# Optimization experiments

Measured on AMD Instinct MI355X. Metric: run time of the kernel, lower is better.

Reference implementation:

```python
import jax, jax.numpy as jnp
import numpy as np

SLOPE = 25.0   # snntorch surrogate.fast_sigmoid default slope
THR = 1.0      # snntorch Leaky default threshold
NUM_STEPS = 100

# fast_sigmoid surrogate spike: heaviside fwd, 1/(slope|x|+1)^2 bwd
@jax.custom_vjp
def spike(x):
    return (x > 0).astype(x.dtype)

def _spike_fwd(x):
    return spike(x), x

def _spike_bwd(x, g):
    return (g / (SLOPE * jnp.abs(x) + 1.0) ** 2,)

spike.defvjp(_spike_fwd, _spike_bwd)


def setup_inputs() -> dict:
    key = jax.random.key(0)
    ks = jax.random.split(key, 5)
    B, D_in, D_h, D_out = 512, 784, 2048, 10
    x = jax.random.normal(ks[0], (B, D_in), dtype=jnp.float32)
    W1 = jax.random.normal(ks[1], (D_h, D_in), dtype=jnp.float32) / np.sqrt(D_in).astype(np.float32)
    b1 = jax.random.normal(ks[2], (D_h,), dtype=jnp.float32) * 0.01
    W2 = jax.random.normal(ks[3], (D_out, D_h), dtype=jnp.float32) / np.sqrt(D_h).astype(np.float32)
    b2 = jax.random.normal(ks[4], (D_out,), dtype=jnp.float32) * 0.01
    beta1 = jnp.asarray(0.9, dtype=jnp.float32)  # learn_beta=True -> parameter
    beta2 = jnp.asarray(0.9, dtype=jnp.float32)
    return {"x": x, "W1": W1, "b1": b1, "W2": W2, "b2": b2, "beta1": beta1, "beta2": beta2}


def reference(x, W1, b1, W2, b2, beta1, beta2):
    dtype = x.dtype
    B = x.shape[0]
    Dh = W1.shape[0]
    Do = W2.shape[0]
    # fc1(x) is loop-invariant in the original (x constant across steps) -> hoist
    cur1 = x @ W1.T + b1                       # [B, Dh]
    b1c = jnp.clip(beta1, 0.0, 1.0)            # snntorch clamps beta in forward
    b2c = jnp.clip(beta2, 0.0, 1.0)
    mem1_0 = jnp.zeros((B, Dh), dtype)         # init_leaky -> 0
    mem2_0 = jnp.zeros((B, Do), dtype)

    def step(carry, _):
        mem1, mem2 = carry
        # snntorch Leaky (reset_mechanism='subtract'):
        # reset_t = detached heaviside(mem_{t-1} - thr); mem_t = beta*mem_{t-1} + cur - reset*thr
        reset1 = jax.lax.stop_gradient((mem1 > THR).astype(dtype))
        mem1 = b1c * mem1 + cur1 - reset1 * THR
        spk1 = spike(mem1 - THR)               # [B, Dh]
        cur2 = spk1 @ W2.T + b2                # [B, Do]
        reset2 = jax.lax.stop_gradient((mem2 > THR).astype(dtype))
        mem2 = b2c * mem2 + cur2 - reset2 * THR
        spk2 = spike(mem2 - THR)
        return (mem1, mem2), spk2

    _, spk2_rec = jax.lax.scan(step, (mem1_0, mem2_0), None, length=NUM_STEPS)  # [T, B, Do]
    # snn_res_step_num == snn_num_steps -> mean over all steps
    stk_mean = jnp.mean(spk2_rec, axis=0)      # [B, Do]
    return jax.nn.softmax(stk_mean, axis=1)
```

## Files before the change

### kernel.cpp

```cpp
#include <hip/hip_runtime.h>
#include <cstdint>

typedef unsigned int u32;
typedef unsigned short u16;
typedef unsigned long long u64;
typedef __attribute__((ext_vector_type(4))) float f32x4;
typedef __attribute__((ext_vector_type(8))) short s16x8;

#define D_IN   784
#define D_H    2048
#define D_O    10
#define T_STEPS 100

static __device__ __forceinline__ u16 f2bf_rn(float f) {
  u32 u = __float_as_uint(f);
  u32 r = u + 0x7FFFu + ((u >> 16) & 1u);
  return (u16)(r >> 16);
}
static __device__ __forceinline__ float bf2f(u16 h) {
  return __uint_as_float(((u32)h) << 16);
}

static __device__ __forceinline__ void packpair(float f0, float f1,
                                                u32& o0, u32& o1, u32& o2) {
  u32 u0 = __float_as_uint(f0), u1 = __float_as_uint(f1);
  o0 = (u0 >> 16) | (u1 & 0xFFFF0000u);
  float r0 = __fsub_rn(f0, __uint_as_float(u0 & 0xFFFF0000u));
  float r1 = __fsub_rn(f1, __uint_as_float(u1 & 0xFFFF0000u));
  u32 v0 = __float_as_uint(r0), v1 = __float_as_uint(r1);
  o1 = (v0 >> 16) | (v1 & 0xFFFF0000u);
  float s0 = __fsub_rn(r0, __uint_as_float(v0 & 0xFFFF0000u));
  float s1 = __fsub_rn(r1, __uint_as_float(v1 & 0xFFFF0000u));
  o2 = (__float_as_uint(s0) >> 16) | (__float_as_uint(s1) & 0xFFFF0000u);
}

__global__ __launch_bounds__(256) void k_prep_w2(const float* __restrict__ W2,
                                                 u32* __restrict__ Phi,
                                                 u32* __restrict__ Plo) {
  int t = blockIdx.x * 256 + threadIdx.x;
  if (t >= 64 * 64) return;
  int kb = t >> 6, l = t & 63;
  int o = l & 15;
  int kbase = kb * 32 + ((l >> 4) << 3);
  u32 hw[4], lw[4];
#pragma unroll
  for (int p = 0; p < 4; ++p) {
    u32 hp = 0, lp = 0;
#pragma unroll
    for (int q = 0; q < 2; ++q) {
      float f = (o < D_O) ? W2[o * D_H + kbase + 2 * p + q] : 0.0f;
      u16 h = f2bf_rn(f);
      float rr = __fsub_rn(f, bf2f(h));
      u16 lo = f2bf_rn(rr);
      hp |= ((u32)h) << (16 * q);
      lp |= ((u32)lo) << (16 * q);
    }
    hw[p] = hp; lw[p] = lp;
  }
  int base = (kb * 64 + l) * 4;
#pragma unroll
  for (int p = 0; p < 4; ++p) { Phi[base + p] = hw[p]; Plo[base + p] = lw[p]; }
}

__global__ __launch_bounds__(512) void k_fgemm(const float* __restrict__ x,
                                               const float* __restrict__ W1,
                                               const float* __restrict__ b1,
                                               float* __restrict__ cur1) {
  __shared__ uint4 As[3][4][64];
  __shared__ uint4 Bs[3][4][64];
  const int tid = threadIdx.x, wave = tid >> 6, lane = tid & 63;
  const int id = blockIdx.x;
  const int sub = id >> 3;
  const int mb = sub >> 2;
  const int nb = (id & 7) * 4 + (sub & 3);
  const int wm = wave >> 1, wn = wave & 1;
  const int st = tid & 255;
  const int srow = st >> 2, skq = st & 3;
  const int sfrag = srow >> 4;
  const int slane = skq * 16 + (srow & 15);
  const bool isA = (tid < 256);
  const float* srcrow = isA ? (x  + (size_t)(mb * 64 + srow) * D_IN)
                            : (W1 + (size_t)(nb * 64 + srow) * D_IN);
  f32x4 acc0 = {0.f, 0.f, 0.f, 0.f}, acc1 = {0.f, 0.f, 0.f, 0.f};
  float e[8];
  {
    const int kg = skq * 8;
    float4 v0 = *(const float4*)(srcrow + kg);
    float4 v1 = *(const float4*)(srcrow + kg + 4);
    e[0] = v0.x; e[1] = v0.y; e[2] = v0.z; e[3] = v0.w;
    e[4] = v1.x; e[5] = v1.y; e[6] = v1.z; e[7] = v1.w;
  }
  for (int kb = 0; kb < 25; ++kb) {
    u32 w0[4], w1[4], w2[4];
#pragma unroll
    for (int p = 0; p < 4; ++p) packpair(e[2 * p], e[2 * p + 1], w0[p], w1[p], w2[p]);
    __syncthreads();
    if (isA) {
      As[0][sfrag][slane] = make_uint4(w0[0], w0[1], w0[2], w0[3]);
      As[1][sfrag][slane] = make_uint4(w1[0], w1[1], w1[2], w1[3]);
      As[2][sfrag][slane] = make_uint4(w2[0], w2[1], w2[2], w2[3]);
    } else {
      Bs[0][sfrag][slane] = make_uint4(w0[0], w0[1], w0[2], w0[3]);
      Bs[1][sfrag][slane] = make_uint4(w1[0], w1[1], w1[2], w1[3]);
      Bs[2][sfrag][slane] = make_uint4(w2[0], w2[1], w2[2], w2[3]);
    }
    __syncthreads();
    if (kb < 24) {
      const int kg = (kb + 1) * 32 + skq * 8;
      if (kg < D_IN) {
        float4 v0 = *(const float4*)(srcrow + kg);
        float4 v1 = *(const float4*)(srcrow + kg + 4);
        e[0] = v0.x; e[1] = v0.y; e[2] = v0.z; e[3] = v0.w;
        e[4] = v1.x; e[5] = v1.y; e[6] = v1.z; e[7] = v1.w;
      } else {
#pragma unroll
        for (int q = 0; q < 8; ++q) e[q] = 0.0f;
      }
    }
    s16x8 A0 = __builtin_bit_cast(s16x8, As[0][wm][lane]);
    s16x8 A1 = __builtin_bit_cast(s16x8, As[1][wm][lane]);
    s16x8 A2 = __builtin_bit_cast(s16x8, As[2][wm][lane]);
    {
      s16x8 B0 = __builtin_bit_cast(s16x8, Bs[0][wn * 2][lane]);
      s16x8 B1 = __builtin_bit_cast(s16x8, Bs[1][wn * 2][lane]);
      s16x8 B2 = __builtin_bit_cast(s16x8, Bs[2][wn * 2][lane]);
      acc0 = __builtin_amdgcn_mfma_f32_16x16x32_bf16(A0, B0, acc0, 0, 0, 0);
      acc0 = __builtin_amdgcn_mfma_f32_16x16x32_bf16(A0, B1, acc0, 0, 0, 0);
      acc0 = __builtin_amdgcn_mfma_f32_16x16x32_bf16(A1, B0, acc0, 0, 0, 0);
      acc0 = __builtin_amdgcn_mfma_f32_16x16x32_bf16(A1, B1, acc0, 0, 0, 0);
      acc0 = __builtin_amdgcn_mfma_f32_16x16x32_bf16(A0, B2, acc0, 0, 0, 0);
      acc0 = __builtin_amdgcn_mfma_f32_16x16x32_bf16(A2, B0, acc0, 0, 0, 0);
    }
    {
      s16x8 B0 = __builtin_bit_cast(s16x8, Bs[0][wn * 2 + 1][lane]);
      s16x8 B1 = __builtin_bit_cast(s16x8, Bs[1][wn * 2 + 1][lane]);
      s16x8 B2 = __builtin_bit_cast(s16x8, Bs[2][wn * 2 + 1][lane]);
      acc1 = __builtin_amdgcn_mfma_f32_16x16x32_bf16(A0, B0, acc1, 0, 0, 0);
      acc1 = __builtin_amdgcn_mfma_f32_16x16x32_bf16(A0, B1, acc1, 0, 0, 0);
      acc1 = __builtin_amdgcn_mfma_f32_16x16x32_bf16(A1, B0, acc1, 0, 0, 0);
      acc1 = __builtin_amdgcn_mfma_f32_16x16x32_bf16(A1, B1, acc1, 0, 0, 0);
      acc1 = __builtin_amdgcn_mfma_f32_16x16x32_bf16(A0, B2, acc1, 0, 0, 0);
      acc1 = __builtin_amdgcn_mfma_f32_16x16x32_bf16(A2, B0, acc1, 0, 0, 0);
    }
  }
  const int col = lane & 15, rb = (lane >> 4) * 4;
  {
    const int gcol = nb * 64 + (wn * 2) * 16 + col;
    const float bv = b1[gcol];
#pragma unroll
    for (int r = 0; r < 4; ++r)
      cur1[(size_t)(mb * 64 + wm * 16 + rb + r) * D_H + gcol] = acc0[r] + bv;
  }
  {
    const int gcol = nb * 64 + (wn * 2 + 1) * 16 + col;
    const float bv = b1[gcol];
#pragma unroll
    for (int r = 0; r < 4; ++r)
      cur1[(size_t)(mb * 64 + wm * 16 + rb + r) * D_H + gcol] = acc1[r] + bv;
  }
}

__global__ __launch_bounds__(512) void k_snn3(const float* __restrict__ cur1,
                                              const u32* __restrict__ Phi,
                                              const u32* __restrict__ Plo,
                                              const float* __restrict__ b2,
                                              const float* __restrict__ beta1p,
                                              const float* __restrict__ beta2p,
                                              float* __restrict__ out) {
  __shared__ __align__(16) u32 bits[112][66];
  __shared__ float c2[112][18];
  const int b = blockIdx.x;
  const int tid = threadIdx.x;
  const int wave = tid >> 6, lane = tid & 63;
  const float b1c = fminf(fmaxf(beta1p[0], 0.0f), 1.0f);
  const float b2c = fminf(fmaxf(beta2p[0], 0.0f), 1.0f);

  for (int idx = tid; idx < 12 * 66; idx += 512) bits[100 + idx / 66][idx % 66] = 0;

  float cv[4], memv[4], spf[4];
#pragma unroll
  for (int j = 0; j < 4; ++j) {
    cv[j] = cur1[(size_t)b * D_H + j * 512 + tid];
    memv[j] = 0.0f; spf[j] = 0.0f;
  }
  for (int t = 0; t < T_STEPS; ++t) {
    u64 msk[4];
#pragma unroll
    for (int j = 0; j < 4; ++j) {
      float m = __fmul_rn(b1c, memv[j]);
      m = __fadd_rn(m, cv[j]);
      m = __fsub_rn(m, spf[j]);
      bool sp = (m > 1.0f);
      msk[j] = __ballot(sp);
      spf[j] = sp ? 1.0f : 0.0f;
      memv[j] = m;
    }
    if (lane == 0) {
      u64* rowp = (u64*)&bits[t][0];
      rowp[0 * 8 + wave] = msk[0];
      rowp[1 * 8 + wave] = msk[1];
      rowp[2 * 8 + wave] = msk[2];
      rowp[3 * 8 + wave] = msk[3];
    }
  }
  __syncthreads();

  if (wave < 7) {
    f32x4 acc = {0.f, 0.f, 0.f, 0.f};
    const int row0 = wave * 16 + (lane & 15);
    const int shift = (lane >> 4) * 8;
    for (int kb = 0; kb < 64; ++kb) {
      const uint4 bh = *(const uint4*)(Phi + (size_t)(kb * 64 + lane) * 4);
      const uint4 bl = *(const uint4*)(Plo + (size_t)(kb * 64 + lane) * 4);
      u32 w8 = (bits[row0][kb] >> shift) & 0xFFu;
      u32 u = w8 | (w8 << 15);
      uint4 a0u;
      ((u32*)&a0u)[0] = ( u        & 0x00010001u) * 0x3F80u;
      ((u32*)&a0u)[1] = ((u >> 2)  & 0x00010001u) * 0x3F80u;
      ((u32*)&a0u)[2] = ((u >> 4)  & 0x00010001u) * 0x3F80u;
      ((u32*)&a0u)[3] = ((u >> 6)  & 0x00010001u) * 0x3F80u;
      s16x8 a   = __builtin_bit_cast(s16x8, a0u);
      s16x8 bhi = __builtin_bit_cast(s16x8, bh);
      s16x8 blo = __builtin_bit_cast(s16x8, bl);
      acc = __builtin_amdgcn_mfma_f32_16x16x32_bf16(a, bhi, acc, 0, 0, 0);
      acc = __builtin_amdgcn_mfma_f32_16x16x32_bf16(a, blo, acc, 0, 0, 0);
    }
    const int colw = lane & 15, rbase = (lane >> 4) * 4;
#pragma unroll
    for (int r = 0; r < 4; ++r) c2[wave * 16 + rbase + r][colw] = acc[r];
  }
  __syncthreads();

  if (tid < 16) {
    const int o = tid;
    const bool valid = (o < D_O);
    const float bb = valid ? b2[o] : 0.0f;
    float m2 = 0.0f; bool s2 = false; int cnt = 0;
    for (int t0 = 0; t0 < T_STEPS; t0 += 10) {
      float cc[10];
#pragma unroll
      for (int i = 0; i < 10; ++i) cc[i] = c2[t0 + i][o];
#pragma unroll
      for (int i = 0; i < 10; ++i) {
        float cI = __fadd_rn(cc[i], bb);
        float m = __fadd_rn(__fmul_rn(b2c, m2), cI);
        if (s2) m = __fsub_rn(m, 1.0f);
        s2 = (m > 1.0f);
        m2 = m;
        cnt += s2 ? 1 : 0;
      }
    }
    float mean = valid ? ((float)cnt / 100.0f) : -1e30f;
    float mx = mean;
#pragma unroll
    for (int i = 8; i >= 1; i >>= 1) mx = fmaxf(mx, __shfl_xor(mx, i, 16));
    float e = valid ? expf(mean - mx) : 0.0f;
    float s = e;
#pragma unroll
    for (int i = 8; i >= 1; i >>= 1) s = __fadd_rn(s, __shfl_xor(s, i, 16));
    if (valid) out[(size_t)b * D_O + o] = e / s;
  }
}

extern "C" void kernel_launch(void* const* d_in, const int* in_sizes, int n_in,
                              void* d_out, int out_size, void* d_ws, size_t ws_size,
                              hipStream_t stream) {
  const float* x     = (const float*)d_in[0];
  const float* W1    = (const float*)d_in[1];
  const float* b1    = (const float*)d_in[2];
  const float* W2    = (const float*)d_in[3];
  const float* b2    = (const float*)d_in[4];
  const float* beta1 = (const float*)d_in[5];
  const float* beta2 = (const float*)d_in[6];
  float* out = (float*)d_out;

  char* ws = (char*)d_ws;
  float* cur1 = (float*)ws;
  u32*   Phi  = (u32*)(ws + 4194304);
  u32*   Plo  = (u32*)(ws + 4259840);

  hipLaunchKernelGGL(k_prep_w2, dim3(16), dim3(256), 0, stream, W2, Phi, Plo);
  hipLaunchKernelGGL(k_fgemm, dim3(256), dim3(512), 0, stream, x, W1, b1, cur1);
  hipLaunchKernelGGL(k_snn3, dim3(512), dim3(512), 0, stream,
                     cur1, Phi, Plo, b2, beta1, beta2, out);
}
```

Baseline: 69.87 us.

## Double-buffer fc1 GEMM LDS, replicate packed W2 copies, batch W2 loads

The fc1 GEMM now double-buffers its shared-memory tiles, so packing and storing the next k-slice overlaps with the MFMAs on the current one, and each iteration needs one barrier instead of two. The W2 prep kernel writes 16 replicated copies of the packed hi/lo weights, and each SNN block reads the copy selected by its block index. This spreads L2 and channel contention across blocks that would otherwise all read the same small buffer. The SNN matmul loop also issues four k-blocks of weight loads before consuming them, which raises memory-level parallelism at the cost of more registers, more LDS and a larger workspace.

Measured after the change: 67.26 us. 1.04x faster.

```diff
diff --git a/kernel.cpp b/kernel.cpp
--- a/kernel.cpp
+++ b/kernel.cpp
@@ -11,6 +11,7 @@
 #define D_H    2048
 #define D_O    10
 #define T_STEPS 100
+#define NCOPY  16
 
 static __device__ __forceinline__ u16 f2bf_rn(float f) {
   u32 u = __float_as_uint(f);
@@ -37,8 +38,9 @@
 __global__ __launch_bounds__(256) void k_prep_w2(const float* __restrict__ W2,
                                                  u32* __restrict__ Phi,
                                                  u32* __restrict__ Plo) {
-  int t = blockIdx.x * 256 + threadIdx.x;
-  if (t >= 64 * 64) return;
+  const int blk = blockIdx.x;
+  const int copy = blk >> 4;
+  int t = (blk & 15) * 256 + threadIdx.x;
   int kb = t >> 6, l = t & 63;
   int o = l & 15;
   int kbase = kb * 32 + ((l >> 4) << 3);
@@ -57,7 +59,7 @@
     }
     hw[p] = hp; lw[p] = lp;
   }
-  int base = (kb * 64 + l) * 4;
+  int base = (copy << 15) + (kb * 64 + l) * 4;
 #pragma unroll
   for (int p = 0; p < 4; ++p) { Phi[base + p] = hw[p]; Plo[base + p] = lw[p]; }
 }
@@ -66,8 +68,8 @@
                                                const float* __restrict__ W1,
                                                const float* __restrict__ b1,
                                                float* __restrict__ cur1) {
-  __shared__ uint4 As[3][4][64];
-  __shared__ uint4 Bs[3][4][64];
+  __shared__ uint4 As[2][3][4][64];
+  __shared__ uint4 Bs[2][3][4][64];
   const int tid = threadIdx.x, wave = tid >> 6, lane = tid & 63;
   const int id = blockIdx.x;
   const int sub = id >> 3;
@@ -90,21 +92,23 @@
     e[0] = v0.x; e[1] = v0.y; e[2] = v0.z; e[3] = v0.w;
     e[4] = v1.x; e[5] = v1.y; e[6] = v1.z; e[7] = v1.w;
   }
+  {
+    u32 w0[4], w1[4], w2[4];
+#pragma unroll
+    for (int p = 0; p < 4; ++p) packpair(e[2 * p], e[2 * p + 1], w0[p], w1[p], w2[p]);
+    if (isA) {
+      As[0][0][sfrag][slane] = make_uint4(w0[0], w0[1], w0[2], w0[3]);
+      As[0][1][sfrag][slane] = make_uint4(w1[0], w1[1], w1[2], w1[3]);
+      As[0][2][sfrag][slane] = make_uint4(w2[0], w2[1], w2[2], w2[3]);
+    } else {
+      Bs[0][0][sfrag][slane] = make_uint4(w0[0], w0[1], w0[2], w0[3]);
+      Bs[0][1][sfrag][slane] = make_uint4(w1[0], w1[1], w1[2], w1[3]);
+      Bs[0][2][sfrag][slane] = make_uint4(w2[0], w2[1], w2[2], w2[3]);
+    }
+  }
+  __syncthreads();
   for (int kb = 0; kb < 25; ++kb) {
-    u32 w0[4], w1[4], w2[4];
-#pragma unroll
-    for (int p = 0; p < 4; ++p) packpair(e[2 * p], e[2 * p + 1], w0[p], w1[p], w2[p]);
-    __syncthreads();
-    if (isA) {
-      As[0][sfrag][slane] = make_uint4(w0[0], w0[1], w0[2], w0[3]);
-      As[1][sfrag][slane] = make_uint4(w1[0], w1[1], w1[2], w1[3]);
-      As[2][sfrag][slane] = make_uint4(w2[0], w2[1], w2[2], w2[3]);
-    } else {
-      Bs[0][sfrag][slane] = make_uint4(w0[0], w0[1], w0[2], w0[3]);
-      Bs[1][sfrag][slane] = make_uint4(w1[0], w1[1], w1[2], w1[3]);
-      Bs[2][sfrag][slane] = make_uint4(w2[0], w2[1], w2[2], w2[3]);
-    }
-    __syncthreads();
+    const int cur = kb & 1, nxt = cur ^ 1;
     if (kb < 24) {
       const int kg = (kb + 1) * 32 + skq * 8;
       if (kg < D_IN) {
@@ -117,13 +121,13 @@
         for (int q = 0; q < 8; ++q) e[q] = 0.0f;
       }
     }
-    s16x8 A0 = __builtin_bit_cast(s16x8, As[0][wm][lane]);
-    s16x8 A1 = __builtin_bit_cast(s16x8, As[1][wm][lane]);
-    s16x8 A2 = __builtin_bit_cast(s16x8, As[2][wm][lane]);
+    s16x8 A0 = __builtin_bit_cast(s16x8, As[cur][0][wm][lane]);
+    s16x8 A1 = __builtin_bit_cast(s16x8, As[cur][1][wm][lane]);
+    s16x8 A2 = __builtin_bit_cast(s16x8, As[cur][2][wm][lane]);
     {
-      s16x8 B0 = __builtin_bit_cast(s16x8, Bs[0][wn * 2][lane]);
-      s16x8 B1 = __builtin_bit_cast(s16x8, Bs[1][wn * 2][lane]);
-      s16x8 B2 = __builtin_bit_cast(s16x8, Bs[2][wn * 2][lane]);
+      s16x8 B0 = __builtin_bit_cast(s16x8, Bs[cur][0][wn * 2][lane]);
+      s16x8 B1 = __builtin_bit_cast(s16x8, Bs[cur][1][wn * 2][lane]);
+      s16x8 B2 = __builtin_bit_cast(s16x8, Bs[cur][2][wn * 2][lane]);
       acc0 = __builtin_amdgcn_mfma_f32_16x16x32_bf16(A0, B0, acc0, 0, 0, 0);
       acc0 = __builtin_amdgcn_mfma_f32_16x16x32_bf16(A0, B1, acc0, 0, 0, 0);
       acc0 = __builtin_amdgcn_mfma_f32_16x16x32_bf16(A1, B0, acc0, 0, 0, 0);
@@ -132,9 +136,9 @@
       acc0 = __builtin_amdgcn_mfma_f32_16x16x32_bf16(A2, B0, acc0, 0, 0, 0);
     }
     {
-      s16x8 B0 = __builtin_bit_cast(s16x8, Bs[0][wn * 2 + 1][lane]);
-      s16x8 B1 = __builtin_bit_cast(s16x8, Bs[1][wn * 2 + 1][lane]);
-      s16x8 B2 = __builtin_bit_cast(s16x8, Bs[2][wn * 2 + 1][lane]);
+      s16x8 B0 = __builtin_bit_cast(s16x8, Bs[cur][0][wn * 2 + 1][lane]);
+      s16x8 B1 = __builtin_bit_cast(s16x8, Bs[cur][1][wn * 2 + 1][lane]);
+      s16x8 B2 = __builtin_bit_cast(s16x8, Bs[cur][2][wn * 2 + 1][lane]);
       acc1 = __builtin_amdgcn_mfma_f32_16x16x32_bf16(A0, B0, acc1, 0, 0, 0);
       acc1 = __builtin_amdgcn_mfma_f32_16x16x32_bf16(A0, B1, acc1, 0, 0, 0);
       acc1 = __builtin_amdgcn_mfma_f32_16x16x32_bf16(A1, B0, acc1, 0, 0, 0);
@@ -142,6 +146,21 @@
       acc1 = __builtin_amdgcn_mfma_f32_16x16x32_bf16(A0, B2, acc1, 0, 0, 0);
       acc1 = __builtin_amdgcn_mfma_f32_16x16x32_bf16(A2, B0, acc1, 0, 0, 0);
     }
+    if (kb < 24) {
+      u32 w0[4], w1[4], w2[4];
+#pragma unroll
+      for (int p = 0; p < 4; ++p) packpair(e[2 * p], e[2 * p + 1], w0[p], w1[p], w2[p]);
+      if (isA) {
+        As[nxt][0][sfrag][slane] = make_uint4(w0[0], w0[1], w0[2], w0[3]);
+        As[nxt][1][sfrag][slane] = make_uint4(w1[0], w1[1], w1[2], w1[3]);
+        As[nxt][2][sfrag][slane] = make_uint4(w2[0], w2[1], w2[2], w2[3]);
+      } else {
+        Bs[nxt][0][sfrag][slane] = make_uint4(w0[0], w0[1], w0[2], w0[3]);
+        Bs[nxt][1][sfrag][slane] = make_uint4(w1[0], w1[1], w1[2], w1[3]);
+        Bs[nxt][2][sfrag][slane] = make_uint4(w2[0], w2[1], w2[2], w2[3]);
+      }
+    }
+    __syncthreads();
   }
   const int col = lane & 15, rb = (lane >> 4) * 4;
   {
@@ -160,7 +179,7 @@
   }
 }
 
-__global__ __launch_bounds__(512) void k_snn3(const float* __restrict__ cur1,
+__global__ __launch_bounds__(512) void k_snn4(const float* __restrict__ cur1,
                                               const u32* __restrict__ Phi,
                                               const u32* __restrict__ Plo,
                                               const float* __restrict__ b2,
@@ -206,24 +225,33 @@
   __syncthreads();
 
   if (wave < 7) {
+    const u32* PhiB = Phi + ((size_t)(b & (NCOPY - 1)) << 15);
+    const u32* PloB = Plo + ((size_t)(b & (NCOPY - 1)) << 15);
     f32x4 acc = {0.f, 0.f, 0.f, 0.f};
     const int row0 = wave * 16 + (lane & 15);
     const int shift = (lane >> 4) * 8;
-    for (int kb = 0; kb < 64; ++kb) {
-      const uint4 bh = *(const uint4*)(Phi + (size_t)(kb * 64 + lane) * 4);
-      const uint4 bl = *(const uint4*)(Plo + (size_t)(kb * 64 + lane) * 4);
-      u32 w8 = (bits[row0][kb] >> shift) & 0xFFu;
-      u32 u = w8 | (w8 << 15);
-      uint4 a0u;
-      ((u32*)&a0u)[0] = ( u        & 0x00010001u) * 0x3F80u;
-      ((u32*)&a0u)[1] = ((u >> 2)  & 0x00010001u) * 0x3F80u;
-      ((u32*)&a0u)[2] = ((u >> 4)  & 0x00010001u) * 0x3F80u;
-      ((u32*)&a0u)[3] = ((u >> 6)  & 0x00010001u) * 0x3F80u;
-      s16x8 a   = __builtin_bit_cast(s16x8, a0u);
-      s16x8 bhi = __builtin_bit_cast(s16x8, bh);
-      s16x8 blo = __builtin_bit_cast(s16x8, bl);
-      acc = __builtin_amdgcn_mfma_f32_16x16x32_bf16(a, bhi, acc, 0, 0, 0);
-      acc = __builtin_amdgcn_mfma_f32_16x16x32_bf16(a, blo, acc, 0, 0, 0);
+    for (int kg = 0; kg < 64; kg += 4) {
+      uint4 bh[4], bl[4];
+#pragma unroll
+      for (int i = 0; i < 4; ++i) {
+        bh[i] = *(const uint4*)(PhiB + (size_t)(kg + i) * 256 + lane * 4);
+        bl[i] = *(const uint4*)(PloB + (size_t)(kg + i) * 256 + lane * 4);
+      }
+#pragma unroll
+      for (int i = 0; i < 4; ++i) {
+        u32 w8 = (bits[row0][kg + i] >> shift) & 0xFFu;
+        u32 u = w8 | (w8 << 15);
+        uint4 a0u;
+        ((u32*)&a0u)[0] = ( u        & 0x00010001u) * 0x3F80u;
+        ((u32*)&a0u)[1] = ((u >> 2)  & 0x00010001u) * 0x3F80u;
+        ((u32*)&a0u)[2] = ((u >> 4)  & 0x00010001u) * 0x3F80u;
+        ((u32*)&a0u)[3] = ((u >> 6)  & 0x00010001u) * 0x3F80u;
+        s16x8 a   = __builtin_bit_cast(s16x8, a0u);
+        s16x8 bhi = __builtin_bit_cast(s16x8, bh[i]);
+        s16x8 blo = __builtin_bit_cast(s16x8, bl[i]);
+        acc = __builtin_amdgcn_mfma_f32_16x16x32_bf16(a, bhi, acc, 0, 0, 0);
+        acc = __builtin_amdgcn_mfma_f32_16x16x32_bf16(a, blo, acc, 0, 0, 0);
+      }
     }
     const int colw = lane & 15, rbase = (lane >> 4) * 4;
 #pragma unroll
@@ -277,10 +305,10 @@
   char* ws = (char*)d_ws;
   float* cur1 = (float*)ws;
   u32*   Phi  = (u32*)(ws + 4194304);
-  u32*   Plo  = (u32*)(ws + 4259840);
-
-  hipLaunchKernelGGL(k_prep_w2, dim3(16), dim3(256), 0, stream, W2, Phi, Plo);
+  u32*   Plo  = (u32*)(ws + 6291456);
+
+  hipLaunchKernelGGL(k_prep_w2, dim3(256), dim3(256), 0, stream, W2, Phi, Plo);
   hipLaunchKernelGGL(k_fgemm, dim3(256), dim3(512), 0, stream, x, W1, b1, cur1);
-  hipLaunchKernelGGL(k_snn3, dim3(512), dim3(512), 0, stream,
+  hipLaunchKernelGGL(k_snn4, dim3(512), dim3(512), 0, stream,
                      cur1, Phi, Plo, b2, beta1, beta2, out);
 }
```
